# Kernel optimization log

Hardware: AMD Instinct MI355X
Metric: run time of the kernel (lower is better)

## Reference

```python
import jax, jax.numpy as jnp
import numpy as np

D_MODEL = 1024
N_HEADS = 16
HEAD_DIM = D_MODEL // N_HEADS


def setup_inputs() -> dict:
    key = jax.random.key(0)
    ks = jax.random.split(key, 5)
    B, T = 4, 2048
    x = jax.random.normal(ks[0], (B, T, D_MODEL), dtype=jnp.float32)
    s_in = 1.0 / np.sqrt(D_MODEL)
    W_qkv = jax.random.normal(ks[1], (D_MODEL, 3 * D_MODEL), dtype=jnp.float32) * s_in
    b_qkv = jnp.zeros((3 * D_MODEL,), dtype=jnp.float32)
    W_proj = jax.random.normal(ks[2], (D_MODEL, D_MODEL), dtype=jnp.float32) * s_in
    b_proj = jnp.zeros((D_MODEL,), dtype=jnp.float32)
    return {"x": x, "W_qkv": W_qkv, "b_qkv": b_qkv, "W_proj": W_proj, "b_proj": b_proj}


def reference(x, W_qkv, b_qkv, W_proj, b_proj):
    B, T, C = x.shape
    qkv = x @ W_qkv + b_qkv                       # [B, T, 3C]
    q, k, v = jnp.split(qkv, 3, axis=-1)
    def heads(t):  # [B, T, C] -> [B, H, T, Dh]
        return t.reshape(B, T, N_HEADS, HEAD_DIM).transpose(0, 2, 1, 3)
    q, k, v = heads(q), heads(k), heads(v)
    scale = 1.0 / np.sqrt(HEAD_DIM)
    att = jnp.einsum('bhqd,bhkd->bhqk', q, k) * scale   # [B, H, T, T]
    causal = jnp.tril(jnp.ones((T, T), dtype=bool))
    att = jnp.where(causal, att, -jnp.inf)
    att = jax.nn.softmax(att, axis=-1)
    out = jnp.einsum('bhqk,bhkd->bhqd', att, v)          # [B, H, T, Dh]
    out = out.transpose(0, 2, 1, 3).reshape(B, T, C)
    return out @ W_proj + b_proj
```

## Files before the change

### kernel.cpp

```cpp
#include <hip/hip_runtime.h>
#include <hip/hip_bf16.h>

#define NH 16
#define HD 64
#define T_SEQ 2048
#define DM 1024

typedef __attribute__((ext_vector_type(8))) short short8;
typedef __attribute__((ext_vector_type(4))) short sh4;
typedef __attribute__((ext_vector_type(4))) float f32x4;
typedef __attribute__((ext_vector_type(16))) float f32x16;
typedef unsigned short ushort;

static __device__ __forceinline__ ushort f2bf(float f) {
    union { float f; unsigned int u; } c; c.f = f;
    unsigned int r = (c.u + 0x7fffu + ((c.u >> 16) & 1u)) >> 16;
    return (ushort)r;
}

static __device__ __forceinline__ void gload16(const ushort* g, ushort* l) {
    __builtin_amdgcn_global_load_lds(
        (const __attribute__((address_space(1))) void*)(const void*)g,
        (__attribute__((address_space(3))) void*)(void*)l, 16, 0, 0);
}

__global__ __launch_bounds__(256) void conv_bf16(const float* __restrict__ src,
                                                 ushort* __restrict__ dst) {
    int i = blockIdx.x * 256 + threadIdx.x;
    const float* s = src + (size_t)i * 8;
    float4 a = *(const float4*)(s);
    float4 b = *(const float4*)(s + 4);
    short8 o;
    o[0] = f2bf(a.x); o[1] = f2bf(a.y); o[2] = f2bf(a.z); o[3] = f2bf(a.w);
    o[4] = f2bf(b.x); o[5] = f2bf(b.y); o[6] = f2bf(b.z); o[7] = f2bf(b.w);
    *(short8*)(dst + (size_t)i * 8) = o;
}

__global__ __launch_bounds__(256) void transpose_w(const float* __restrict__ W,
                                                   ushort* __restrict__ Wt, int N) {
    __shared__ float Ts[64][65];
    const int n0 = blockIdx.x * 64, k0 = blockIdx.y * 64;
    const int tid = threadIdx.x;
    const int cg = tid & 15, r4 = tid >> 4;
    #pragma unroll
    for (int i = 0; i < 4; ++i) {
        int r = r4 + i * 16;
        float4 v = *(const float4*)(W + (size_t)(k0 + r) * N + n0 + cg * 4);
        Ts[r][cg * 4 + 0] = v.x; Ts[r][cg * 4 + 1] = v.y;
        Ts[r][cg * 4 + 2] = v.z; Ts[r][cg * 4 + 3] = v.w;
    }
    __syncthreads();
    #pragma unroll
    for (int i = 0; i < 4; ++i) {
        int r = r4 + i * 16;
        sh4 o;
        o[0] = (short)f2bf(Ts[cg * 4 + 0][r]);
        o[1] = (short)f2bf(Ts[cg * 4 + 1][r]);
        o[2] = (short)f2bf(Ts[cg * 4 + 2][r]);
        o[3] = (short)f2bf(Ts[cg * 4 + 3][r]);
        *(sh4*)(Wt + (size_t)(n0 + r) * DM + k0 + cg * 4) = o;
    }
}

static __device__ __forceinline__ void gemm_core(
    const ushort* __restrict__ A, const ushort* __restrict__ Bt,
    ushort* __restrict__ smem, int m0, int n0, f32x4 acc[4][4])
{
    const int tid = threadIdx.x;
    const int wid = tid >> 6, lane = tid & 63;
    const int lr = lane & 15, g = lane >> 4;
    const int wm = wid >> 1, wn = wid & 1;
    const int lrow = lane >> 3, lslot = lane & 7;

    auto stage = [&](int b, int kt) {
        ushort* As = smem + b * 16384;
        ushort* Bs = As + 8192;
        #pragma unroll
        for (int i = 0; i < 4; ++i) {
            const int row = wid * 32 + i * 8 + lrow;
            const int gcol = (lslot ^ (row & 7)) * 8;
            const int ldsoff = (wid * 32 + i * 8) * 64;
            gload16(A  + (size_t)(m0 + row) * DM + kt * 64 + gcol, As + ldsoff);
            gload16(Bt + (size_t)(n0 + row) * DM + kt * 64 + gcol, Bs + ldsoff);
        }
    };

    stage(0, 0);
    #pragma unroll 1
    for (int kt = 0; kt < 16; ++kt) {
        const int cur = kt & 1;
        if (kt < 15) {
            stage(cur ^ 1, kt + 1);
            asm volatile("s_waitcnt vmcnt(8)" ::: "memory");
        } else {
            asm volatile("s_waitcnt vmcnt(0)" ::: "memory");
        }
        __builtin_amdgcn_s_barrier();
        __builtin_amdgcn_sched_barrier(0);
        const ushort* As = smem + cur * 16384;
        const ushort* Bs = As + 8192;
        #pragma unroll
        for (int ks = 0; ks < 2; ++ks) {
            short8 af[4], bfr[4];
            #pragma unroll
            for (int mi = 0; mi < 4; ++mi) {
                int row = wm * 64 + mi * 16 + lr;
                af[mi] = *(const short8*)(As + row * 64 + (((ks * 4 + g) ^ (row & 7)) * 8));
            }
            #pragma unroll
            for (int ni = 0; ni < 4; ++ni) {
                int row = wn * 64 + ni * 16 + lr;
                bfr[ni] = *(const short8*)(Bs + row * 64 + (((ks * 4 + g) ^ (row & 7)) * 8));
            }
            #pragma unroll
            for (int mi = 0; mi < 4; ++mi)
                #pragma unroll
                for (int ni = 0; ni < 4; ++ni)
                    acc[mi][ni] = __builtin_amdgcn_mfma_f32_16x16x32_bf16(af[mi], bfr[ni], acc[mi][ni], 0, 0, 0);
        }
        __builtin_amdgcn_sched_barrier(0);
        __builtin_amdgcn_s_barrier();
    }
}

__global__ __launch_bounds__(256) void qkv_mfma(
    const ushort* __restrict__ Xb, const ushort* __restrict__ Wqt,
    const float* __restrict__ bias,
    ushort* __restrict__ Qb, ushort* __restrict__ Kb, ushort* __restrict__ Vt)
{
    __shared__ __align__(16) ushort smem[32768];
    const int m0 = blockIdx.y * 128;
    const int n0 = blockIdx.x * 128;
    f32x4 acc[4][4] = {};
    gemm_core(Xb, Wqt, smem, m0, n0, acc);

    const int tid = threadIdx.x;
    const int wid = tid >> 6, lane = tid & 63;
    const int lr = lane & 15, g = lane >> 4;
    const int wm = wid >> 1, wn = wid & 1;
    const int which = n0 >> 10;
    const int bq = m0 >> 11;

    if (which < 2) {
        ushort* dst = which ? Kb : Qb;
        const float sc = which ? 1.0f : 0.125f * 1.44269504f;
        #pragma unroll
        for (int ni = 0; ni < 4; ++ni) {
            int nn = n0 + wn * 64 + ni * 16 + lr;
            const float bv = bias[nn];
            const int hh = (nn & 1023) >> 6, dd = nn & 63;
            const size_t hb = ((size_t)(bq * NH + hh)) * T_SEQ;
            #pragma unroll
            for (int mi = 0; mi < 4; ++mi)
                #pragma unroll
                for (int r = 0; r < 4; ++r) {
                    int t = (m0 + wm * 64 + mi * 16 + g * 4 + r) & 2047;
                    dst[(hb + t) * HD + dd] = f2bf((acc[mi][ni][r] + bv) * sc);
                }
        }
    } else {
        __syncthreads();
        ushort* Ct = smem;
        #pragma unroll
        for (int ni = 0; ni < 4; ++ni) {
            int lcol = wn * 64 + ni * 16 + lr;
            const float bv = bias[n0 + lcol];
            #pragma unroll
            for (int mi = 0; mi < 4; ++mi)
                #pragma unroll
                for (int r = 0; r < 4; ++r)
                    Ct[(wm * 64 + mi * 16 + g * 4 + r) * 128 + lcol] = f2bf(acc[mi][ni][r] + bv);
        }
        __syncthreads();
        const int dloc = tid >> 1, th = (tid & 1) * 64;
        const int nn = (n0 & 1023) + dloc;
        ushort* dst = Vt + ((size_t)(bq * 1024 + nn)) * T_SEQ + (m0 & 2047) + th;
        #pragma unroll
        for (int e8 = 0; e8 < 8; ++e8) {
            short8 v;
            #pragma unroll
            for (int u = 0; u < 8; ++u) v[u] = (short)Ct[(th + e8 * 8 + u) * 128 + dloc];
            *(short8*)(dst + e8 * 8) = v;
        }
    }
}

__global__ __launch_bounds__(256) void proj_mfma(
    const ushort* __restrict__ AO, const ushort* __restrict__ Wpt,
    const float* __restrict__ bias, float* __restrict__ Y)
{
    __shared__ __align__(16) ushort smem[32768];
    const int m0 = blockIdx.y * 128;
    const int n0 = blockIdx.x * 128;
    f32x4 acc[4][4] = {};
    gemm_core(AO, Wpt, smem, m0, n0, acc);

    const int tid = threadIdx.x;
    const int wid = tid >> 6, lane = tid & 63;
    const int lr = lane & 15, g = lane >> 4;
    const int wm = wid >> 1, wn = wid & 1;
    #pragma unroll
    for (int ni = 0; ni < 4; ++ni) {
        int nn = n0 + wn * 64 + ni * 16 + lr;
        const float bv = bias[nn];
        #pragma unroll
        for (int mi = 0; mi < 4; ++mi)
            #pragma unroll
            for (int r = 0; r < 4; ++r) {
                int m = m0 + wm * 64 + mi * 16 + g * 4 + r;
                Y[(size_t)m * DM + nn] = acc[mi][ni][r] + bv;
            }
    }
}

__global__ __launch_bounds__(256) void attn_mfma(
    const ushort* __restrict__ Qb,
    const ushort* __restrict__ Kb,
    const ushort* __restrict__ Vt,
    ushort* __restrict__ AO)
{
    __shared__ __align__(16) ushort Ks[2][4096];
    __shared__ __align__(16) ushort Vs[2][4096];

    const int bh = blockIdx.x;
    const int j = 15 - blockIdx.y;
    const int tid = threadIdx.x;
    const int wid = tid >> 6;
    const int lane = tid & 63;
    const int ql = lane & 31;
    const int hi = lane >> 5;

    const ushort* Kg = Kb + (size_t)bh * T_SEQ * HD;
    const ushort* Vg = Vt + (size_t)bh * HD * T_SEQ;

    const int srow = tid >> 3;
    const int sco = (tid & 7) * 8;
    const int ssw = sco ^ ((srow & 7) << 3);
    const int sdst0 = srow * 64 + ssw;
    const int sdst1 = (srow + 32) * 64 + ssw;

    const int b = bh >> 4, h = bh & 15;
    ushort* AOg = AO + (size_t)b * T_SEQ * DM + h * HD;

    const int q0 = j * 128;
    const int qlo = q0 + wid * 32;
    const int ntiles = 2 * j + 2;

    short8 qb[4];
    {
        const ushort* Qg = Qb + ((size_t)bh * T_SEQ + qlo) * HD;
        #pragma unroll
        for (int ds = 0; ds < 4; ++ds)
            qb[ds] = *(const short8*)(Qg + (size_t)ql * HD + ds * 16 + hi * 8);
    }

    f32x16 po[2] = {};
    float lp = 0.f;

    short8 rk0, rk1, rv0, rv1;
    rk0 = *(const short8*)(Kg + (size_t)srow * HD + sco);
    rk1 = *(const short8*)(Kg + (size_t)(srow + 32) * HD + sco);
    rv0 = *(const short8*)(Vg + (size_t)srow * T_SEQ + sco);
    rv1 = *(const short8*)(Vg + (size_t)(srow + 32) * T_SEQ + sco);
    *(short8*)(&Ks[0][sdst0]) = rk0;  *(short8*)(&Ks[0][sdst1]) = rk1;
    *(short8*)(&Vs[0][sdst0]) = rv0;  *(short8*)(&Vs[0][sdst1]) = rv1;
    {
        const int nk0 = 64;
        rk0 = *(const short8*)(Kg + (size_t)(nk0 + srow) * HD + sco);
        rk1 = *(const short8*)(Kg + (size_t)(nk0 + srow + 32) * HD + sco);
        rv0 = *(const short8*)(Vg + (size_t)srow * T_SEQ + nk0 + sco);
        rv1 = *(const short8*)(Vg + (size_t)(srow + 32) * T_SEQ + nk0 + sco);
    }
    __syncthreads();

    for (int tt = 0; tt < ntiles; ++tt) {
        const int k0 = tt * 64;
        const int cur = tt & 1;
        if (tt + 1 < ntiles) {
            const int nxt = cur ^ 1;
            *(short8*)(&Ks[nxt][sdst0]) = rk0;  *(short8*)(&Ks[nxt][sdst1]) = rk1;
            *(short8*)(&Vs[nxt][sdst0]) = rv0;  *(short8*)(&Vs[nxt][sdst1]) = rv1;
            if (tt + 2 < ntiles) {
                const int nk0 = (tt + 2) * 64;
                rk0 = *(const short8*)(Kg + (size_t)(nk0 + srow) * HD + sco);
                rk1 = *(const short8*)(Kg + (size_t)(nk0 + srow + 32) * HD + sco);
                rv0 = *(const short8*)(Vg + (size_t)srow * T_SEQ + nk0 + sco);
                rv1 = *(const short8*)(Vg + (size_t)(srow + 32) * T_SEQ + nk0 + sco);
            }
        }

        if (k0 <= qlo + 31) {
            const ushort* ksb = Ks[cur];
            const ushort* vsb = Vs[cur];

            short8 vf[2][4];
            #pragma unroll
            for (int db = 0; db < 2; ++db)
                #pragma unroll
                for (int sl = 0; sl < 4; ++sl) {
                    int row = db * 32 + ql;
                    int slot = (sl * 2 + hi) ^ (row & 7);
                    vf[db][sl] = *(const short8*)(&vsb[row * 64 + slot * 8]);
                }

            f32x16 sp[2] = {};
            __builtin_amdgcn_s_setprio(1);
            #pragma unroll
            for (int kb = 0; kb < 2; ++kb) {
                #pragma unroll
                for (int ds = 0; ds < 4; ++ds) {
                    int row = kb * 32 + ql;
                    int slot = (ds * 2 + hi) ^ (row & 7);
                    short8 kf = *(const short8*)(&ksb[row * 64 + slot * 8]);
                    sp[kb] = __builtin_amdgcn_mfma_f32_32x32x16_bf16(kf, qb[ds], sp[kb], 0, 0, 0);
                }
            }
            __builtin_amdgcn_s_setprio(0);

            if (k0 + 63 > qlo) {
                #pragma unroll
                for (int kb = 0; kb < 2; ++kb) {
                    const int lim = qlo + ql - k0 - kb * 32 - 4 * hi;
                    #pragma unroll
                    for (int r = 0; r < 16; ++r) {
                        const int c = (r & 3) + 8 * (r >> 2);
                        sp[kb][r] = (c <= lim) ? sp[kb][r] : -INFINITY;
                    }
                }
            }

            float rs = 0.f;
            #pragma unroll
            for (int kb = 0; kb < 2; ++kb)
                #pragma unroll
                for (int r = 0; r < 16; ++r) {
                    float p;
                    asm("v_exp_f32 %0, %1" : "=v"(p) : "v"(sp[kb][r]));
                    sp[kb][r] = p;
                    rs += p;
                }
            lp += rs;

            #pragma unroll
            for (int kb = 0; kb < 2; ++kb) {
                #pragma unroll
                for (int ks16 = 0; ks16 < 2; ++ks16) {
                    unsigned int x0, x1, y0, y1;
                    const int rb0 = ks16 * 2, rb1 = ks16 * 2 + 1;
                    asm("v_cvt_pk_bf16_f32 %0, %1, %2" : "=v"(x0)
                        : "v"(sp[kb][4 * rb0 + 0]), "v"(sp[kb][4 * rb0 + 1]));
                    asm("v_cvt_pk_bf16_f32 %0, %1, %2" : "=v"(x1)
                        : "v"(sp[kb][4 * rb0 + 2]), "v"(sp[kb][4 * rb0 + 3]));
                    asm("v_cvt_pk_bf16_f32 %0, %1, %2" : "=v"(y0)
                        : "v"(sp[kb][4 * rb1 + 0]), "v"(sp[kb][4 * rb1 + 1]));
                    asm("v_cvt_pk_bf16_f32 %0, %1, %2" : "=v"(y1)
                        : "v"(sp[kb][4 * rb1 + 2]), "v"(sp[kb][4 * rb1 + 3]));
                    asm("v_permlane32_swap_b32 %0, %1" : "+v"(x0), "+v"(y0));
                    asm("v_permlane32_swap_b32 %0, %1" : "+v"(x1), "+v"(y1));
                    union { unsigned int w[4]; short8 s8; } pb;
                    pb.w[0] = x0; pb.w[1] = x1; pb.w[2] = y0; pb.w[3] = y1;
                    const int sl = kb * 2 + ks16;
                    __builtin_amdgcn_s_setprio(1);
                    po[0] = __builtin_amdgcn_mfma_f32_32x32x16_bf16(vf[0][sl], pb.s8, po[0], 0, 0, 0);
                    po[1] = __builtin_amdgcn_mfma_f32_32x32x16_bf16(vf[1][sl], pb.s8, po[1], 0, 0, 0);
                    __builtin_amdgcn_s_setprio(0);
                }
            }
        }
        __syncthreads();
    }

    lp += __shfl_xor(lp, 32);
    const float inv = 1.f / lp;
    const int q = qlo + ql;
    #pragma unroll
    for (int db = 0; db < 2; ++db) {
        #pragma unroll
        for (int rb = 0; rb < 4; ++rb) {
            unsigned int w0, w1;
            float f0 = po[db][4 * rb + 0] * inv, f1 = po[db][4 * rb + 1] * inv;
            float f2 = po[db][4 * rb + 2] * inv, f3 = po[db][4 * rb + 3] * inv;
            asm("v_cvt_pk_bf16_f32 %0, %1, %2" : "=v"(w0) : "v"(f0), "v"(f1));
            asm("v_cvt_pk_bf16_f32 %0, %1, %2" : "=v"(w1) : "v"(f2), "v"(f3));
            uint2 wv; wv.x = w0; wv.y = w1;
            *(uint2*)(AOg + (size_t)q * DM + db * 32 + 8 * rb + 4 * hi) = wv;
        }
    }
}

extern "C" void kernel_launch(void* const* d_in, const int* in_sizes, int n_in,
                              void* d_out, int out_size, void* d_ws, size_t ws_size,
                              hipStream_t stream) {
    const float* x      = (const float*)d_in[0];
    const float* W_qkv  = (const float*)d_in[1];
    const float* b_qkv  = (const float*)d_in[2];
    const float* W_proj = (const float*)d_in[3];
    const float* b_proj = (const float*)d_in[4];
    float* out = (float*)d_out;

    const size_t perbuf = (size_t)4 * NH * T_SEQ * HD;
    ushort* Qb  = (ushort*)d_ws;
    ushort* Kb  = Qb + perbuf;
    ushort* Vt  = Kb + perbuf;
    ushort* AO  = Vt + perbuf;
    ushort* Wqt = AO;
    ushort* Wpt = Qb;
    ushort* Xb  = (ushort*)d_out;

    hipLaunchKernelGGL(conv_bf16, dim3(4096), dim3(256), 0, stream, x, Xb);
    hipLaunchKernelGGL(transpose_w, dim3(48, 16), dim3(256), 0, stream, W_qkv, Wqt, 3 * DM);
    hipLaunchKernelGGL(qkv_mfma, dim3(24, 64), dim3(256), 0, stream,
                       Xb, Wqt, b_qkv, Qb, Kb, Vt);
    hipLaunchKernelGGL(attn_mfma, dim3(64, 16), dim3(256), 0, stream,
                       Qb, Kb, Vt, AO);
    hipLaunchKernelGGL(transpose_w, dim3(16, 16), dim3(256), 0, stream, W_proj, Wpt, DM);
    hipLaunchKernelGGL(proj_mfma, dim3(8, 64), dim3(256), 0, stream,
                       AO, Wpt, b_proj, out);
}
```

Baseline: 159.5 us.

## Use 256x128 tiles with K=32 double buffering for the QKV GEMM

Adds a new GEMM core for the QKV projection that computes 256x128 output tiles per block. It uses a K-step of 32 with two LDS buffers and a new swizzle, and each wave reuses its B fragments across 8 M-subtiles. This raises arithmetic intensity per LDS read and halves the grid to 768 blocks. The V-transpose epilogue now runs in two passes through the smaller shared buffer. The cost is more accumulator registers, which may lower occupancy, and fewer blocks to spread across the CUs.

```diff
diff --git a/kernel.cpp b/kernel.cpp
--- a/kernel.cpp
+++ b/kernel.cpp
@@ -123,16 +123,78 @@
     }
 }
 
+static __device__ __forceinline__ void gemm_core_256(
+    const ushort* __restrict__ A, const ushort* __restrict__ Bt,
+    ushort* __restrict__ smem, int m0, int n0, f32x4 acc[8][4])
+{
+    const int tid = threadIdx.x;
+    const int wid = tid >> 6, lane = tid & 63;
+    const int lr = lane & 15, g = lane >> 4;
+    const int wm = wid >> 1, wn = wid & 1;
+    const int lrow16 = lane >> 2, lslot4 = lane & 3;
+
+    auto stage = [&](int b, int kt) {
+        ushort* As = smem + b * 12288;
+        ushort* Bs = As + 8192;
+        #pragma unroll
+        for (int i = 0; i < 4; ++i) {
+            const int rbase = wid * 64 + i * 16;
+            const int row = rbase + lrow16;
+            const int ks = lslot4 ^ ((row >> 1) & 3);
+            gload16(A + (size_t)(m0 + row) * DM + kt * 32 + ks * 8, As + rbase * 32);
+        }
+        #pragma unroll
+        for (int i = 0; i < 2; ++i) {
+            const int rbase = wid * 32 + i * 16;
+            const int row = rbase + lrow16;
+            const int ks = lslot4 ^ ((row >> 1) & 3);
+            gload16(Bt + (size_t)(n0 + row) * DM + kt * 32 + ks * 8, Bs + rbase * 32);
+        }
+    };
+
+    stage(0, 0);
+    #pragma unroll 1
+    for (int kt = 0; kt < 32; ++kt) {
+        const int cur = kt & 1;
+        if (kt < 31) {
+            stage(cur ^ 1, kt + 1);
+            asm volatile("s_waitcnt vmcnt(6)" ::: "memory");
+        } else {
+            asm volatile("s_waitcnt vmcnt(0)" ::: "memory");
+        }
+        __builtin_amdgcn_s_barrier();
+        __builtin_amdgcn_sched_barrier(0);
+        const ushort* As = smem + cur * 12288;
+        const ushort* Bs = As + 8192;
+        short8 bfr[4];
+        #pragma unroll
+        for (int ni = 0; ni < 4; ++ni) {
+            int row = wn * 64 + ni * 16 + lr;
+            bfr[ni] = *(const short8*)(Bs + row * 32 + ((g ^ ((row >> 1) & 3)) * 8));
+        }
+        #pragma unroll
+        for (int mi = 0; mi < 8; ++mi) {
+            int row = wm * 128 + mi * 16 + lr;
+            short8 af = *(const short8*)(As + row * 32 + ((g ^ ((row >> 1) & 3)) * 8));
+            #pragma unroll
+            for (int ni = 0; ni < 4; ++ni)
+                acc[mi][ni] = __builtin_amdgcn_mfma_f32_16x16x32_bf16(af, bfr[ni], acc[mi][ni], 0, 0, 0);
+        }
+        __builtin_amdgcn_sched_barrier(0);
+        __builtin_amdgcn_s_barrier();
+    }
+}
+
 __global__ __launch_bounds__(256) void qkv_mfma(
     const ushort* __restrict__ Xb, const ushort* __restrict__ Wqt,
     const float* __restrict__ bias,
     ushort* __restrict__ Qb, ushort* __restrict__ Kb, ushort* __restrict__ Vt)
 {
-    __shared__ __align__(16) ushort smem[32768];
-    const int m0 = blockIdx.y * 128;
+    __shared__ __align__(16) ushort smem[24576];
+    const int m0 = blockIdx.y * 256;
     const int n0 = blockIdx.x * 128;
-    f32x4 acc[4][4] = {};
-    gemm_core(Xb, Wqt, smem, m0, n0, acc);
+    f32x4 acc[8][4] = {};
+    gemm_core_256(Xb, Wqt, smem, m0, n0, acc);
 
     const int tid = threadIdx.x;
     const int wid = tid >> 6, lane = tid & 63;
@@ -151,36 +213,41 @@
             const int hh = (nn & 1023) >> 6, dd = nn & 63;
             const size_t hb = ((size_t)(bq * NH + hh)) * T_SEQ;
             #pragma unroll
-            for (int mi = 0; mi < 4; ++mi)
+            for (int mi = 0; mi < 8; ++mi)
                 #pragma unroll
                 for (int r = 0; r < 4; ++r) {
-                    int t = (m0 + wm * 64 + mi * 16 + g * 4 + r) & 2047;
+                    int t = (m0 + wm * 128 + mi * 16 + g * 4 + r) & 2047;
                     dst[(hb + t) * HD + dd] = f2bf((acc[mi][ni][r] + bv) * sc);
                 }
         }
     } else {
-        __syncthreads();
         ushort* Ct = smem;
-        #pragma unroll
-        for (int ni = 0; ni < 4; ++ni) {
-            int lcol = wn * 64 + ni * 16 + lr;
-            const float bv = bias[n0 + lcol];
-            #pragma unroll
-            for (int mi = 0; mi < 4; ++mi)
-                #pragma unroll
-                for (int r = 0; r < 4; ++r)
-                    Ct[(wm * 64 + mi * 16 + g * 4 + r) * 128 + lcol] = f2bf(acc[mi][ni][r] + bv);
-        }
-        __syncthreads();
         const int dloc = tid >> 1, th = (tid & 1) * 64;
         const int nn = (n0 & 1023) + dloc;
-        ushort* dst = Vt + ((size_t)(bq * 1024 + nn)) * T_SEQ + (m0 & 2047) + th;
-        #pragma unroll
-        for (int e8 = 0; e8 < 8; ++e8) {
-            short8 v;
-            #pragma unroll
-            for (int u = 0; u < 8; ++u) v[u] = (short)Ct[(th + e8 * 8 + u) * 128 + dloc];
-            *(short8*)(dst + e8 * 8) = v;
+        #pragma unroll 1
+        for (int p = 0; p < 2; ++p) {
+            __syncthreads();
+            if (wm == p) {
+                #pragma unroll
+                for (int ni = 0; ni < 4; ++ni) {
+                    int lcol = wn * 64 + ni * 16 + lr;
+                    const float bv = bias[n0 + lcol];
+                    #pragma unroll
+                    for (int mi = 0; mi < 8; ++mi)
+                        #pragma unroll
+                        for (int r = 0; r < 4; ++r)
+                            Ct[(mi * 16 + g * 4 + r) * 128 + lcol] = f2bf(acc[mi][ni][r] + bv);
+                }
+            }
+            __syncthreads();
+            ushort* dst = Vt + ((size_t)(bq * 1024 + nn)) * T_SEQ + (m0 & 2047) + p * 128 + th;
+            #pragma unroll
+            for (int e8 = 0; e8 < 8; ++e8) {
+                short8 v;
+                #pragma unroll
+                for (int u = 0; u < 8; ++u) v[u] = (short)Ct[(th + e8 * 8 + u) * 128 + dloc];
+                *(short8*)(dst + e8 * 8) = v;
+            }
         }
     }
 }
@@ -409,7 +476,7 @@
 
     hipLaunchKernelGGL(conv_bf16, dim3(4096), dim3(256), 0, stream, x, Xb);
     hipLaunchKernelGGL(transpose_w, dim3(48, 16), dim3(256), 0, stream, W_qkv, Wqt, 3 * DM);
-    hipLaunchKernelGGL(qkv_mfma, dim3(24, 64), dim3(256), 0, stream,
+    hipLaunchKernelGGL(qkv_mfma, dim3(24, 32), dim3(256), 0, stream,
                        Xb, Wqt, b_qkv, Qb, Kb, Vt);
     hipLaunchKernelGGL(attn_mfma, dim3(64, 16), dim3(256), 0, stream,
                        Qb, Kb, Vt, AO);
```

New measurement: 180.7 us. 1.13x slower.
